# Optimization experiments

Measured on AMD Instinct MI355X. Metric: run time of the kernel, lower is better.

Reference implementation:

```python
import jax, jax.numpy as jnp
import numpy as np

B, T, C = 4, 2048, 1024
H, DK, DV = 16, 64, 64


def setup_inputs() -> dict:
    key = jax.random.key(0)
    ks = jax.random.split(key, 12)
    s = 1.0 / np.sqrt(C)
    inp = {
        "Q": jax.random.normal(ks[0], (B, T, C), jnp.float32),
        "K": jax.random.normal(ks[1], (B, T, C), jnp.float32),
        "V": jax.random.normal(ks[2], (B, T, C), jnp.float32),
        # causal mask: True (==1) means masked out
        "mask": jnp.broadcast_to(jnp.triu(jnp.ones((T, T), bool), k=1), (B, 1, T, T)),
        "Wq": jax.random.uniform(ks[3], (C, H * DK), jnp.float32, -s, s),
        "bq": jax.random.uniform(ks[4], (H * DK,), jnp.float32, -s, s),
        "Wk": jax.random.uniform(ks[5], (C, H * DK), jnp.float32, -s, s),
        "bk": jax.random.uniform(ks[6], (H * DK,), jnp.float32, -s, s),
        "Wv": jax.random.uniform(ks[7], (C, H * DV), jnp.float32, -s, s),
        "bv": jax.random.uniform(ks[8], (H * DV,), jnp.float32, -s, s),
        "Wo": jax.random.uniform(ks[9], (H * DV, C), jnp.float32, -s, s),
        "bo": jax.random.uniform(ks[10], (C,), jnp.float32, -s, s),
    }
    return inp


def _split(x, d):
    b, t, _ = x.shape
    return x.reshape(b, t, H, d).transpose(0, 2, 1, 3)  # (B,H,T,d)


def reference(Q, K, V, mask, Wq, bq, Wk, bk, Wv, bv, Wo, bo):
    Qh = _split(Q @ Wq + bq, DK)
    Kh = _split(K @ Wk + bk, DK)
    Vh = _split(V @ Wv + bv, DV)
    scores = jnp.einsum('bhqd,bhkd->bhqk', Qh, Kh) / jnp.sqrt(jnp.float32(DK))
    scores = jnp.where(mask, -jnp.inf, scores)
    attn = jax.nn.softmax(scores, axis=-1)
    out = jnp.einsum('bhqk,bhkd->bhqd', attn, Vh)
    out = out.transpose(0, 2, 1, 3).reshape(B, T, H * DV)
    return out @ Wo + bo
```

## Files before the change

kernel.cpp:

```cpp
#include <hip/hip_runtime.h>
#include <stdint.h>

#define BATCH 4
#define SEQ   2048
#define CH    1024
#define NH    16
#define HD    64

#define QSCALE 0.18033688011112042f

#define GM 8192
#define GN 1024
#define GK 1024

typedef __attribute__((ext_vector_type(8))) short bf16x8;
typedef __attribute__((ext_vector_type(4))) float f32x4;

__device__ inline unsigned short f2bf(float f) {
    unsigned u = __float_as_uint(f);
    u += 0x7fff + ((u >> 16) & 1);
    return (unsigned short)(u >> 16);
}

__device__ inline float fast_exp2(float x) {
    float r;
    asm("v_exp_f32 %0, %1" : "=v"(r) : "v"(x));
    return r;
}

__device__ inline unsigned cvt_pk_bf16(float lo, float hi) {
    unsigned r;
    asm("v_cvt_pk_bf16_f32 %0, %1, %2" : "=v"(r) : "v"(lo), "v"(hi));
    return r;
}

__device__ inline void gld_lds16(const void* g, void* l) {
    __builtin_amdgcn_global_load_lds((const __attribute__((address_space(1))) void*)g,
                                     (__attribute__((address_space(3))) void*)l,
                                     16, 0, 0);
}

__global__ __launch_bounds__(256) void prep_k(
    const float* __restrict__ Q, const float* __restrict__ K, const float* __restrict__ V,
    unsigned short* __restrict__ Qbf, unsigned short* __restrict__ Kbf, unsigned short* __restrict__ Vbf,
    const float* __restrict__ Wq, const float* __restrict__ Wk,
    const float* __restrict__ Wv, const float* __restrict__ Wo,
    unsigned short* __restrict__ WqT, unsigned short* __restrict__ WkT,
    unsigned short* __restrict__ WvT, unsigned short* __restrict__ WoT)
{
    const int bid = blockIdx.x;
    if (bid < 12288) {
        const int j     = bid >> 12;
        const int local = bid & 4095;
        const float* in = (j == 0) ? Q : (j == 1) ? K : V;
        unsigned short* out = (j == 0) ? Qbf : (j == 1) ? Kbf : Vbf;
        const int i = (local * 256 + threadIdx.x) * 8;
        f32x4 a = *(const f32x4*)(in + i);
        f32x4 b = *(const f32x4*)(in + i + 4);
        union { bf16x8 v; unsigned short s[8]; } o;
        o.s[0] = f2bf(a[0]); o.s[1] = f2bf(a[1]); o.s[2] = f2bf(a[2]); o.s[3] = f2bf(a[3]);
        o.s[4] = f2bf(b[0]); o.s[5] = f2bf(b[1]); o.s[6] = f2bf(b[2]); o.s[7] = f2bf(b[3]);
        *(bf16x8*)(out + i) = o.v;
    } else {
        __shared__ float tile[32][33];
        const int idx   = bid - 12288;
        const int j     = idx >> 10;
        const int local = idx & 1023;
        const float* W = (j == 0) ? Wq : (j == 1) ? Wk : (j == 2) ? Wv : Wo;
        unsigned short* Wt = (j == 0) ? WqT : (j == 1) ? WkT : (j == 2) ? WvT : WoT;
        const int bx = (local & 31) * 32;
        const int by = (local >> 5) * 32;
        const int tx = threadIdx.x & 31;
        const int ty = threadIdx.x >> 5;
#pragma unroll
        for (int i = 0; i < 32; i += 8)
            tile[ty + i][tx] = W[(size_t)(by + ty + i) * CH + bx + tx];
        __syncthreads();
#pragma unroll
        for (int i = 0; i < 32; i += 8)
            Wt[(size_t)(bx + ty + i) * CH + by + tx] = f2bf(tile[tx][ty + i]);
    }
}

__global__ __launch_bounds__(256, 2)
void qkv_gemm(const unsigned short* __restrict__ Qbf, const unsigned short* __restrict__ Kbf,
              const unsigned short* __restrict__ Vbf,
              const unsigned short* __restrict__ WqT, const unsigned short* __restrict__ WkT,
              const unsigned short* __restrict__ WvT,
              const float* __restrict__ bq, const float* __restrict__ bk,
              const float* __restrict__ bv,
              unsigned short* __restrict__ Qhb, unsigned short* __restrict__ Khb,
              unsigned short* __restrict__ Vtb)
{
    __shared__ unsigned short As[128 * 64];
    __shared__ unsigned short Bs[128 * 64];
    const int job = blockIdx.y;
    const unsigned short* A   = (job == 0) ? Qbf : (job == 1) ? Kbf : Vbf;
    const unsigned short* Bt  = (job == 0) ? WqT : (job == 1) ? WkT : WvT;
    const float* bias         = (job == 0) ? bq  : (job == 1) ? bk  : bv;
    unsigned short* outp      = (job == 0) ? Qhb : (job == 1) ? Khb : Vtb;
    const float oscale        = (job == 0) ? QSCALE : 1.0f;

    const int tid  = threadIdx.x;
    const int lane = tid & 63;
    const int w    = tid >> 6;
    const int nbn  = GN >> 7;
    const int nbm  = GM >> 7;
    const int xcd  = blockIdx.x & 7;
    const int idx  = blockIdx.x >> 3;
    const int mb   = xcd * (nbm >> 3) + idx / nbn;
    const int nb   = idx % nbn;
    const int m0   = mb << 7;
    const int n0   = nb << 7;
    const int wrow = (w >> 1) << 6;
    const int wcol = (w & 1) << 6;
    const int lr   = lane & 15;
    const int lg   = lane >> 4;

    f32x4 acc[4][4] = {};

    for (int k0 = 0; k0 < GK; k0 += 64) {
#pragma unroll
        for (int i = 0; i < 4; ++i) {
            int chunk = i * 256 + tid;
            int row = chunk >> 3;
            int c8  = (chunk & 7) << 3;
            gld_lds16(A  + (size_t)(m0 + row) * GK + k0 + c8, (char*)As + chunk * 16);
            gld_lds16(Bt + (size_t)(n0 + row) * GK + k0 + c8, (char*)Bs + chunk * 16);
        }
        __syncthreads();
#pragma unroll
        for (int kk = 0; kk < 2; ++kk) {
            bf16x8 af[4], bfr[4];
#pragma unroll
            for (int f = 0; f < 4; ++f)
                af[f] = *(const bf16x8*)(As + (wrow + f * 16 + lr) * 64 + kk * 32 + lg * 8);
#pragma unroll
            for (int f = 0; f < 4; ++f)
                bfr[f] = *(const bf16x8*)(Bs + (wcol + f * 16 + lr) * 64 + kk * 32 + lg * 8);
#pragma unroll
            for (int i = 0; i < 4; ++i)
#pragma unroll
                for (int j = 0; j < 4; ++j)
                    acc[i][j] = __builtin_amdgcn_mfma_f32_16x16x32_bf16(af[i], bfr[j], acc[i][j], 0, 0, 0);
        }
        __syncthreads();
    }

    float bvals[4];
#pragma unroll
    for (int j = 0; j < 4; ++j) bvals[j] = bias[n0 + wcol + j * 16 + lr];

    if (job < 2) {
#pragma unroll
        for (int i = 0; i < 4; ++i) {
            const int mbase = m0 + wrow + i * 16 + lg * 4;
#pragma unroll
            for (int j = 0; j < 4; ++j) {
                const int n = n0 + wcol + j * 16 + lr;
                const int h = n >> 6, d = n & 63;
#pragma unroll
                for (int r = 0; r < 4; ++r) {
                    const int m = mbase + r;
                    const int b = m >> 11, t = m & 2047;
                    outp[((size_t)(b * NH + h) * SEQ + t) * HD + d] = f2bf((acc[i][j][r] + bvals[j]) * oscale);
                }
            }
        }
    } else {
#pragma unroll
        for (int i = 0; i < 4; ++i) {
            const int mbase = m0 + wrow + i * 16 + lg * 4;
#pragma unroll
            for (int j = 0; j < 4; ++j) {
                const int n = n0 + wcol + j * 16 + lr;
                const int h = n >> 6, d = n & 63;
                const int b = mbase >> 11, t = mbase & 2047;
                union { unsigned short s[4]; uint2 v; } pk;
#pragma unroll
                for (int r = 0; r < 4; ++r) pk.s[r] = f2bf(acc[i][j][r] + bvals[j]);
                *(uint2*)(outp + ((size_t)(b * NH + h) * HD + d) * SEQ + t) = pk.v;
            }
        }
    }
}

__global__ __launch_bounds__(256, 2)
void gemm_out(const unsigned short* __restrict__ A,
              const unsigned short* __restrict__ Bt,
              const float* __restrict__ bias,
              float* __restrict__ out)
{
    __shared__ unsigned short As[128 * 64];
    __shared__ unsigned short Bs[128 * 64];
    const int tid  = threadIdx.x;
    const int lane = tid & 63;
    const int w    = tid >> 6;
    const int nbn  = GN >> 7;
    const int nbm  = GM >> 7;
    const int xcd  = blockIdx.x & 7;
    const int idx  = blockIdx.x >> 3;
    const int mb   = xcd * (nbm >> 3) + idx / nbn;
    const int nb   = idx % nbn;
    const int m0   = mb << 7;
    const int n0   = nb << 7;
    const int wrow = (w >> 1) << 6;
    const int wcol = (w & 1) << 6;
    const int lr   = lane & 15;
    const int lg   = lane >> 4;

    f32x4 acc[4][4] = {};

    for (int k0 = 0; k0 < GK; k0 += 64) {
#pragma unroll
        for (int i = 0; i < 4; ++i) {
            int chunk = i * 256 + tid;
            int row = chunk >> 3;
            int c8  = (chunk & 7) << 3;
            gld_lds16(A  + (size_t)(m0 + row) * GK + k0 + c8, (char*)As + chunk * 16);
            gld_lds16(Bt + (size_t)(n0 + row) * GK + k0 + c8, (char*)Bs + chunk * 16);
        }
        __syncthreads();
#pragma unroll
        for (int kk = 0; kk < 2; ++kk) {
            bf16x8 af[4], bfr[4];
#pragma unroll
            for (int f = 0; f < 4; ++f)
                af[f] = *(const bf16x8*)(As + (wrow + f * 16 + lr) * 64 + kk * 32 + lg * 8);
#pragma unroll
            for (int f = 0; f < 4; ++f)
                bfr[f] = *(const bf16x8*)(Bs + (wcol + f * 16 + lr) * 64 + kk * 32 + lg * 8);
#pragma unroll
            for (int i = 0; i < 4; ++i)
#pragma unroll
                for (int j = 0; j < 4; ++j)
                    acc[i][j] = __builtin_amdgcn_mfma_f32_16x16x32_bf16(af[i], bfr[j], acc[i][j], 0, 0, 0);
        }
        __syncthreads();
    }

    float bvals[4];
#pragma unroll
    for (int j = 0; j < 4; ++j) bvals[j] = bias[n0 + wcol + j * 16 + lr];

#pragma unroll
    for (int i = 0; i < 4; ++i) {
        const int mbase = m0 + wrow + i * 16 + lg * 4;
#pragma unroll
        for (int j = 0; j < 4; ++j) {
            const int n = n0 + wcol + j * 16 + lr;
#pragma unroll
            for (int r = 0; r < 4; ++r)
                out[(size_t)(mbase + r) * GN + n] = acc[i][j][r] + bvals[j];
        }
    }
}

__global__ __launch_bounds__(256, 4)
void attn_k(const unsigned short* __restrict__ Qh,
            const unsigned short* __restrict__ Kh,
            const unsigned short* __restrict__ Vt,
            unsigned short* __restrict__ O) {
    __shared__ unsigned short Ks[2][64 * 64];
    __shared__ unsigned short Vs[2][64 * 64];
    __shared__ unsigned short Ps[4][16 * 64];
    const int bh    = blockIdx.x;
    const int qtile = 31 - blockIdx.y;
    const int q0    = qtile << 6;
    const int tid  = threadIdx.x;
    const int lane = tid & 63;
    const int w    = tid >> 6;
    const int lr   = lane & 15;
    const int lg   = lane >> 4;
    const int qw   = q0 + w * 16;
    unsigned short* Pw = Ps[w];

    bf16x8 vones;
#pragma unroll
    for (int j = 0; j < 8; ++j) vones[j] = (short)0x3F80;

    bf16x8 qf[2];
#pragma unroll
    for (int kk = 0; kk < 2; ++kk)
        qf[kk] = *(const bf16x8*)(Qh + ((size_t)bh * SEQ + qw + lr) * HD + kk * 32 + lg * 8);

    float mrun[4];
    f32x4 oacc[4] = {};
    f32x4 osum = {};
#pragma unroll
    for (int r = 0; r < 4; ++r) mrun[r] = -3e38f;

    const int nkt = qtile + 1;

#define STAGE(KT, B) do {                                                          \
        const int kv_ = (KT) << 6;                                                 \
        _Pragma("unroll")                                                          \
        for (int i_ = 0; i_ < 2; ++i_) {                                           \
            int c_ = i_ * 256 + tid;                                               \
            int row_ = c_ >> 3;                                                    \
            int so_ = (((c_ & 7) ^ (row_ & 7)) << 3);                              \
            gld_lds16(Kh + ((size_t)bh * SEQ + kv_ + row_) * HD + so_,             \
                      (char*)Ks[B] + c_ * 16);                                     \
            gld_lds16(Vt + ((size_t)bh * HD + row_) * SEQ + kv_ + so_,             \
                      (char*)Vs[B] + c_ * 16);                                     \
        }                                                                          \
    } while (0)

    STAGE(0, 0);
    __syncthreads();

    for (int kt = 0; kt < nkt; ++kt) {
        if (kt + 1 < nkt) STAGE(kt + 1, (kt + 1) & 1);
        const unsigned short* Kc = Ks[kt & 1];
        const unsigned short* Vc = Vs[kt & 1];
        const int kv0 = kt << 6;

        {
            f32x4 s[4] = {};
            __builtin_amdgcn_s_setprio(1);
#pragma unroll
            for (int kk = 0; kk < 2; ++kk) {
                const int u = (((kk << 2) | lg) ^ (lr & 7)) << 3;
#pragma unroll
                for (int f = 0; f < 4; ++f) {
                    bf16x8 kb = *(const bf16x8*)(Kc + (f * 16 + lr) * 64 + u);
                    s[f] = __builtin_amdgcn_mfma_f32_16x16x32_bf16(qf[kk], kb, s[f], 0, 0, 0);
                }
            }
            __builtin_amdgcn_s_setprio(0);

            float rmax[4];
#pragma unroll
            for (int r = 0; r < 4; ++r) rmax[r] = -3e38f;
            if (kv0 + 63 <= qw) {
#pragma unroll
                for (int f = 0; f < 4; ++f)
#pragma unroll
                    for (int r = 0; r < 4; ++r) rmax[r] = fmaxf(rmax[r], s[f][r]);
            } else {
#pragma unroll
                for (int f = 0; f < 4; ++f)
#pragma unroll
                    for (int r = 0; r < 4; ++r) {
                        const int q  = qw + lg * 4 + r;
                        const int kv = kv0 + f * 16 + lr;
                        float v = (kv > q) ? -3e38f : s[f][r];
                        s[f][r] = v;
                        rmax[r] = fmaxf(rmax[r], v);
                    }
            }
#pragma unroll
            for (int d = 1; d < 16; d <<= 1)
#pragma unroll
                for (int r = 0; r < 4; ++r)
                    rmax[r] = fmaxf(rmax[r], __shfl_xor(rmax[r], d));

            bool grow = (rmax[0] > mrun[0]) | (rmax[1] > mrun[1]) |
                        (rmax[2] > mrun[2]) | (rmax[3] > mrun[3]);
            if (__any(grow)) {
#pragma unroll
                for (int r = 0; r < 4; ++r) {
                    float mn = fmaxf(mrun[r], rmax[r]);
                    float c  = fast_exp2(mrun[r] - mn);
                    mrun[r]  = mn;
                    osum[r] *= c;
#pragma unroll
                    for (int f = 0; f < 4; ++f) oacc[f][r] *= c;
                }
            }

#pragma unroll
            for (int f = 0; f < 4; ++f)
#pragma unroll
                for (int r = 0; r < 4; ++r)
                    s[f][r] = fast_exp2(s[f][r] - mrun[r]);
#pragma unroll
            for (int f = 0; f < 4; ++f)
#pragma unroll
                for (int rp = 0; rp < 2; ++rp) {
                    unsigned pk = cvt_pk_bf16(s[f][2 * rp], s[f][2 * rp + 1]);
                    const int p0 = lg * 4 + 2 * rp;
                    const int p1 = p0 + 1;
                    Pw[p0 * 64 + ((f * 16 + lr) ^ ((p0 & 7) << 3))] = (unsigned short)pk;
                    Pw[p1 * 64 + ((f * 16 + lr) ^ ((p1 & 7) << 3))] = (unsigned short)(pk >> 16);
                }

            bf16x8 pa[2];
#pragma unroll
            for (int kk = 0; kk < 2; ++kk)
                pa[kk] = *(const bf16x8*)(Pw + lr * 64 + ((((kk << 2) | lg) ^ (lr & 7)) << 3));

            __builtin_amdgcn_s_setprio(1);
#pragma unroll
            for (int kk = 0; kk < 2; ++kk) {
                const int u = (((kk << 2) | lg) ^ (lr & 7)) << 3;
#pragma unroll
                for (int f = 0; f < 4; ++f) {
                    bf16x8 vb = *(const bf16x8*)(Vc + (f * 16 + lr) * 64 + u);
                    oacc[f] = __builtin_amdgcn_mfma_f32_16x16x32_bf16(pa[kk], vb, oacc[f], 0, 0, 0);
                }
                osum = __builtin_amdgcn_mfma_f32_16x16x32_bf16(pa[kk], vones, osum, 0, 0, 0);
            }
            __builtin_amdgcn_s_setprio(0);
        }
        __syncthreads();
    }
#undef STAGE

    const int b = bh >> 4, h = bh & 15;
    float inv[4];
#pragma unroll
    for (int r = 0; r < 4; ++r) inv[r] = 1.0f / osum[r];
#pragma unroll
    for (int f = 0; f < 4; ++f) {
        const int d = f * 16 + lr;
#pragma unroll
        for (int r = 0; r < 4; ++r) {
            const int t = qw + lg * 4 + r;
            O[((size_t)b * SEQ + t) * CH + h * HD + d] = f2bf(oacc[f][r] * inv[r]);
        }
    }
}

extern "C" void kernel_launch(void* const* d_in, const int* in_sizes, int n_in,
                              void* d_out, int out_size, void* d_ws, size_t ws_size,
                              hipStream_t stream) {
    const float* Q  = (const float*)d_in[0];
    const float* K  = (const float*)d_in[1];
    const float* V  = (const float*)d_in[2];
    const float* Wq = (const float*)d_in[4];
    const float* bq = (const float*)d_in[5];
    const float* Wk = (const float*)d_in[6];
    const float* bk = (const float*)d_in[7];
    const float* Wv = (const float*)d_in[8];
    const float* bv = (const float*)d_in[9];
    const float* Wo = (const float*)d_in[10];
    const float* bo = (const float*)d_in[11];
    float* out = (float*)d_out;

    const size_t SZ_ACT = (size_t)BATCH * SEQ * CH;
    const size_t SZ_W   = (size_t)CH * CH;

    char* p = (char*)d_ws;
    unsigned short* Qbf = (unsigned short*)p; p += SZ_ACT * 2;
    unsigned short* Kbf = (unsigned short*)p; p += SZ_ACT * 2;
    unsigned short* Vbf = (unsigned short*)p; p += SZ_ACT * 2;
    unsigned short* WqT = (unsigned short*)p; p += SZ_W * 2;
    unsigned short* WkT = (unsigned short*)p; p += SZ_W * 2;
    unsigned short* WvT = (unsigned short*)p; p += SZ_W * 2;
    unsigned short* WoT = (unsigned short*)p; p += SZ_W * 2;
    unsigned short* Qhb = (unsigned short*)p; p += SZ_ACT * 2;
    unsigned short* Khb = (unsigned short*)p; p += SZ_ACT * 2;
    unsigned short* Vtb = (unsigned short*)p; p += SZ_ACT * 2;
    unsigned short* Ob  = Qbf;

    prep_k<<<16384, 256, 0, stream>>>(Q, K, V, Qbf, Kbf, Vbf,
                                      Wq, Wk, Wv, Wo, WqT, WkT, WvT, WoT);

    qkv_gemm<<<dim3((GM / 128) * (GN / 128), 3), 256, 0, stream>>>(
        Qbf, Kbf, Vbf, WqT, WkT, WvT, bq, bk, bv, Qhb, Khb, Vtb);

    attn_k<<<dim3(BATCH * NH, SEQ / 64), 256, 0, stream>>>(Qhb, Khb, Vtb, Ob);

    gemm_out<<<(GM / 128) * (GN / 128), 256, 0, stream>>>(Ob, WoT, bo, out);
}
```

Baseline: 208.6 us.

## Compute transposed scores so P stays in registers, dropping the LDS round-trip

Swaps the MFMA operands so S^T is computed, giving each lane one query row. The P fragments then feed the PV MFMA directly from registers via 16x16x16 bf16 MFMAs, which removes the per-tile LDS write and read of P. The row-max reduction shrinks to two shuffles and the output is stored as packed 8-byte writes. In exchange the PV product uses twice as many smaller MFMAs, the V reads become 8-byte LDS loads, and the s_setprio hints are dropped.

```diff
diff --git a/kernel.cpp b/kernel.cpp
--- a/kernel.cpp
+++ b/kernel.cpp
@@ -14,6 +14,7 @@
 #define GK 1024
 
 typedef __attribute__((ext_vector_type(8))) short bf16x8;
+typedef __attribute__((ext_vector_type(4))) short bf16x4;
 typedef __attribute__((ext_vector_type(4))) float f32x4;
 
 __device__ inline unsigned short f2bf(float f) {
@@ -33,6 +34,17 @@
     asm("v_cvt_pk_bf16_f32 %0, %1, %2" : "=v"(r) : "v"(lo), "v"(hi));
     return r;
 }
+
+#if __has_builtin(__builtin_amdgcn_mfma_f32_16x16x16bf16_1k)
+__device__ inline void mfma16(f32x4& c, bf16x4 a, bf16x4 b) {
+    c = __builtin_amdgcn_mfma_f32_16x16x16bf16_1k(a, b, c, 0, 0, 0);
+}
+#else
+__device__ inline void mfma16(f32x4& c, bf16x4 a, bf16x4 b) {
+    asm volatile("s_nop 2\n\tv_mfma_f32_16x16x16_bf16 %0, %1, %2, %0"
+                 : "+v"(c) : "v"(a), "v"(b));
+}
+#endif
 
 __device__ inline void gld_lds16(const void* g, void* l) {
     __builtin_amdgcn_global_load_lds((const __attribute__((address_space(1))) void*)g,
@@ -263,7 +275,6 @@
             unsigned short* __restrict__ O) {
     __shared__ unsigned short Ks[2][64 * 64];
     __shared__ unsigned short Vs[2][64 * 64];
-    __shared__ unsigned short Ps[4][16 * 64];
     const int bh    = blockIdx.x;
     const int qtile = 31 - blockIdx.y;
     const int q0    = qtile << 6;
@@ -273,22 +284,20 @@
     const int lr   = lane & 15;
     const int lg   = lane >> 4;
     const int qw   = q0 + w * 16;
-    unsigned short* Pw = Ps[w];
-
-    bf16x8 vones;
-#pragma unroll
-    for (int j = 0; j < 8; ++j) vones[j] = (short)0x3F80;
+    const int swz8 = (lr & 7) << 3;
+
+    bf16x4 ones4;
+#pragma unroll
+    for (int j = 0; j < 4; ++j) ones4[j] = (short)0x3F80;
 
     bf16x8 qf[2];
 #pragma unroll
     for (int kk = 0; kk < 2; ++kk)
         qf[kk] = *(const bf16x8*)(Qh + ((size_t)bh * SEQ + qw + lr) * HD + kk * 32 + lg * 8);
 
-    float mrun[4];
-    f32x4 oacc[4] = {};
+    float mrun = -3e38f;
+    f32x4 ot[4] = {};
     f32x4 osum = {};
-#pragma unroll
-    for (int r = 0; r < 4; ++r) mrun[r] = -3e38f;
 
     const int nkt = qtile + 1;
 
@@ -315,110 +324,75 @@
         const unsigned short* Vc = Vs[kt & 1];
         const int kv0 = kt << 6;
 
-        {
-            f32x4 s[4] = {};
-            __builtin_amdgcn_s_setprio(1);
-#pragma unroll
-            for (int kk = 0; kk < 2; ++kk) {
-                const int u = (((kk << 2) | lg) ^ (lr & 7)) << 3;
-#pragma unroll
-                for (int f = 0; f < 4; ++f) {
-                    bf16x8 kb = *(const bf16x8*)(Kc + (f * 16 + lr) * 64 + u);
-                    s[f] = __builtin_amdgcn_mfma_f32_16x16x32_bf16(qf[kk], kb, s[f], 0, 0, 0);
+        f32x4 s[4] = {};
+#pragma unroll
+        for (int kk = 0; kk < 2; ++kk) {
+            const int u = (((kk << 2) | lg) ^ (lr & 7)) << 3;
+#pragma unroll
+            for (int f = 0; f < 4; ++f) {
+                bf16x8 kb = *(const bf16x8*)(Kc + (f * 16 + lr) * 64 + u);
+                s[f] = __builtin_amdgcn_mfma_f32_16x16x32_bf16(kb, qf[kk], s[f], 0, 0, 0);
+            }
+        }
+
+        float rmax = -3e38f;
+        if (kv0 + 63 <= qw) {
+#pragma unroll
+            for (int f = 0; f < 4; ++f)
+#pragma unroll
+                for (int r = 0; r < 4; ++r) rmax = fmaxf(rmax, s[f][r]);
+        } else {
+            const int q = qw + lr;
+#pragma unroll
+            for (int f = 0; f < 4; ++f)
+#pragma unroll
+                for (int r = 0; r < 4; ++r) {
+                    const int kv = kv0 + f * 16 + lg * 4 + r;
+                    float v = (kv > q) ? -3e38f : s[f][r];
+                    s[f][r] = v;
+                    rmax = fmaxf(rmax, v);
                 }
+        }
+        rmax = fmaxf(rmax, __shfl_xor(rmax, 16));
+        rmax = fmaxf(rmax, __shfl_xor(rmax, 32));
+
+        if (__any(rmax > mrun)) {
+            float mn = fmaxf(mrun, rmax);
+            float c  = fast_exp2(mrun - mn);
+            mrun = mn;
+            osum *= c;
+#pragma unroll
+            for (int dd = 0; dd < 4; ++dd) ot[dd] *= c;
+        }
+
+#pragma unroll
+        for (int f = 0; f < 4; ++f) {
+#pragma unroll
+            for (int r = 0; r < 4; ++r)
+                s[f][r] = fast_exp2(s[f][r] - mrun);
+            union { bf16x4 v; unsigned u[2]; } pb;
+            pb.u[0] = cvt_pk_bf16(s[f][0], s[f][1]);
+            pb.u[1] = cvt_pk_bf16(s[f][2], s[f][3]);
+            mfma16(osum, ones4, pb.v);
+#pragma unroll
+            for (int dd = 0; dd < 4; ++dd) {
+                bf16x4 va = *(const bf16x4*)(Vc + (dd * 16 + lr) * 64 + ((f * 16 + lg * 4) ^ swz8));
+                mfma16(ot[dd], va, pb.v);
             }
-            __builtin_amdgcn_s_setprio(0);
-
-            float rmax[4];
-#pragma unroll
-            for (int r = 0; r < 4; ++r) rmax[r] = -3e38f;
-            if (kv0 + 63 <= qw) {
-#pragma unroll
-                for (int f = 0; f < 4; ++f)
-#pragma unroll
-                    for (int r = 0; r < 4; ++r) rmax[r] = fmaxf(rmax[r], s[f][r]);
-            } else {
-#pragma unroll
-                for (int f = 0; f < 4; ++f)
-#pragma unroll
-                    for (int r = 0; r < 4; ++r) {
-                        const int q  = qw + lg * 4 + r;
-                        const int kv = kv0 + f * 16 + lr;
-                        float v = (kv > q) ? -3e38f : s[f][r];
-                        s[f][r] = v;
-                        rmax[r] = fmaxf(rmax[r], v);
-                    }
-            }
-#pragma unroll
-            for (int d = 1; d < 16; d <<= 1)
-#pragma unroll
-                for (int r = 0; r < 4; ++r)
-                    rmax[r] = fmaxf(rmax[r], __shfl_xor(rmax[r], d));
-
-            bool grow = (rmax[0] > mrun[0]) | (rmax[1] > mrun[1]) |
-                        (rmax[2] > mrun[2]) | (rmax[3] > mrun[3]);
-            if (__any(grow)) {
-#pragma unroll
-                for (int r = 0; r < 4; ++r) {
-                    float mn = fmaxf(mrun[r], rmax[r]);
-                    float c  = fast_exp2(mrun[r] - mn);
-                    mrun[r]  = mn;
-                    osum[r] *= c;
-#pragma unroll
-                    for (int f = 0; f < 4; ++f) oacc[f][r] *= c;
-                }
-            }
-
-#pragma unroll
-            for (int f = 0; f < 4; ++f)
-#pragma unroll
-                for (int r = 0; r < 4; ++r)
-                    s[f][r] = fast_exp2(s[f][r] - mrun[r]);
-#pragma unroll
-            for (int f = 0; f < 4; ++f)
-#pragma unroll
-                for (int rp = 0; rp < 2; ++rp) {
-                    unsigned pk = cvt_pk_bf16(s[f][2 * rp], s[f][2 * rp + 1]);
-                    const int p0 = lg * 4 + 2 * rp;
-                    const int p1 = p0 + 1;
-                    Pw[p0 * 64 + ((f * 16 + lr) ^ ((p0 & 7) << 3))] = (unsigned short)pk;
-                    Pw[p1 * 64 + ((f * 16 + lr) ^ ((p1 & 7) << 3))] = (unsigned short)(pk >> 16);
-                }
-
-            bf16x8 pa[2];
-#pragma unroll
-            for (int kk = 0; kk < 2; ++kk)
-                pa[kk] = *(const bf16x8*)(Pw + lr * 64 + ((((kk << 2) | lg) ^ (lr & 7)) << 3));
-
-            __builtin_amdgcn_s_setprio(1);
-#pragma unroll
-            for (int kk = 0; kk < 2; ++kk) {
-                const int u = (((kk << 2) | lg) ^ (lr & 7)) << 3;
-#pragma unroll
-                for (int f = 0; f < 4; ++f) {
-                    bf16x8 vb = *(const bf16x8*)(Vc + (f * 16 + lr) * 64 + u);
-                    oacc[f] = __builtin_amdgcn_mfma_f32_16x16x32_bf16(pa[kk], vb, oacc[f], 0, 0, 0);
-                }
-                osum = __builtin_amdgcn_mfma_f32_16x16x32_bf16(pa[kk], vones, osum, 0, 0, 0);
-            }
-            __builtin_amdgcn_s_setprio(0);
         }
         __syncthreads();
     }
 #undef STAGE
 
     const int b = bh >> 4, h = bh & 15;
-    float inv[4];
-#pragma unroll
-    for (int r = 0; r < 4; ++r) inv[r] = 1.0f / osum[r];
-#pragma unroll
-    for (int f = 0; f < 4; ++f) {
-        const int d = f * 16 + lr;
-#pragma unroll
-        for (int r = 0; r < 4; ++r) {
-            const int t = qw + lg * 4 + r;
-            O[((size_t)b * SEQ + t) * CH + h * HD + d] = f2bf(oacc[f][r] * inv[r]);
-        }
+    const float inv = 1.0f / osum[0];
+    const int t = qw + lr;
+#pragma unroll
+    for (int dd = 0; dd < 4; ++dd) {
+        union { unsigned short s4[4]; uint2 v; } pk;
+#pragma unroll
+        for (int r = 0; r < 4; ++r) pk.s4[r] = f2bf(ot[dd][r] * inv);
+        *(uint2*)(O + ((size_t)b * SEQ + t) * CH + h * HD + dd * 16 + lg * 4) = pk.v;
     }
 }
 
```

New measurement: 189.2 us. -9.3%, faster.
